# Optimization experiments

Hardware: AMD Instinct MI355X
Metric: run time of the kernel (lower is better)

The kernel has to match this reference:

```python
import jax, jax.numpy as jnp
import numpy as np

B, DIM, L = 16, 1024, 1024
EPS = 1e-12  # F.normalize eps


def l2norm(x, axis=1):
    # torch F.normalize: x / clamp_min(||x||_2, eps)
    n = jnp.sqrt(jnp.sum(x * x, axis=axis, keepdims=True))
    return x / jnp.maximum(n, EPS)


def setup_inputs() -> dict:
    key = jax.random.key(0)
    ks = jax.random.split(key, 8)
    inp = {
        "V": jax.random.normal(ks[0], (B, DIM, L), dtype=jnp.float32),
        "T": jax.random.normal(ks[1], (B, DIM, L), dtype=jnp.float32),
    }
    scale = 1.0 / np.sqrt(DIM)
    names = ["WQ1", "WK1", "WV1", "Wq2", "Wk2", "Wv2"]
    for i, nme in enumerate(names):
        inp[nme] = jax.random.normal(ks[2 + i], (DIM, DIM), dtype=jnp.float32) * scale
    return inp


def reference(V, T, WQ1, WK1, WV1, Wq2, Wk2, Wv2):
    # V, T: [B, dim, L]
    T = l2norm(T, axis=1)                      # normalize over feature dim
    Vt = jnp.swapaxes(V, -2, -1)               # [B, L, dim]
    Tt = jnp.swapaxes(T, -2, -1)               # [B, L, dim]

    relu = jax.nn.relu
    q1 = relu(jnp.einsum('bld,ed->ble', Vt, WQ1))
    k1 = relu(jnp.einsum('bld,ed->ble', Tt, WK1))
    v1 = relu(jnp.einsum('bld,ed->ble', Tt, WV1))
    q2 = relu(jnp.einsum('bld,ed->ble', Tt, Wq2))
    k2 = relu(jnp.einsum('bld,ed->ble', Vt, Wk2))
    v2 = relu(jnp.einsum('bld,ed->ble', Vt, Wv2))

    inv_sqrt_d = 1.0 / jnp.sqrt(jnp.asarray(DIM, dtype=q1.dtype))

    s1 = jnp.einsum('bqd,bkd->bqk', q1, k1) * inv_sqrt_d   # [B, Lv, Lt]
    p1 = jax.nn.softmax(s1, axis=1)                        # softmax over query axis (dim=1)
    w1 = jnp.einsum('bqk,bkd->bqd', p1, v1)                # [B, Lv, dim]
    cV = l2norm(V + jnp.swapaxes(w1, -2, -1), axis=1)      # [B, dim, Lv]

    s2 = jnp.einsum('bqd,bkd->bqk', q2, k2) * inv_sqrt_d   # [B, Lt, Lv]
    p2 = jax.nn.softmax(s2, axis=1)
    w2 = jnp.einsum('bqk,bkd->bqd', p2, v2)                # [B, Lt, dim]
    cT = l2norm(T + jnp.swapaxes(w2, -2, -1), axis=1)      # [B, dim, Lt]

    return l2norm(cV + cT, axis=1)
```

## Files before the change

### kernel.cpp

```cpp
#include <hip/hip_runtime.h>

#define L 1024
#define DIM 1024
#define NB 16

typedef unsigned short u16;
typedef __attribute__((ext_vector_type(4))) float f32x4;
typedef __attribute__((ext_vector_type(8))) short s16x8;

__device__ __forceinline__ float bf2f(u16 x){
  union { unsigned u; float f; } c; c.u = ((unsigned)x) << 16; return c.f;
}
__device__ __forceinline__ u16 f2bf(float f){
  union { float f; unsigned u; } c; c.f = f;
  unsigned r = c.u + 0x7fffu + ((c.u >> 16) & 1u);
  return (u16)(r >> 16);
}
__device__ __forceinline__ void gload_lds16(const void* g, void* l){
  __builtin_amdgcn_global_load_lds(
      (const __attribute__((address_space(1))) void*)g,
      (__attribute__((address_space(3))) void*)l, 16, 0, 0);
}

struct WPtrs { const float* p[6]; };

__global__ __launch_bounds__(256) void k_wconv(WPtrs wp, u16* out){
  long idx = (long)blockIdx.x * blockDim.x + threadIdx.x;
  long base = idx * 4;
  int w = (int)(base >> 20);
  long off = base & ((1 << 20) - 1);
  float4 v = *(const float4*)(wp.p[w] + off);
  ushort4 o;
  o.x = f2bf(v.x); o.y = f2bf(v.y); o.z = f2bf(v.z); o.w = f2bf(v.w);
  *(ushort4*)(out + base) = o;
}

__global__ __launch_bounds__(256) void k_transpose(const float* X, u16* Xt, int bo){
  __shared__ u16 tile[64][68];
  int b = blockIdx.y;
  int d0 = (blockIdx.x >> 4) * 64;
  int l0 = (blockIdx.x & 15) * 64;
  const float* Xb = X + (long)(bo + b) * DIM * L;
  u16* Xtb = Xt + (long)b * L * DIM;
  int q = threadIdx.x & 15, g = threadIdx.x >> 4;
  for (int r = g; r < 64; r += 16){
    float4 v = *(const float4*)(Xb + (long)(d0 + r) * L + l0 + q * 4);
    ushort4 h; h.x = f2bf(v.x); h.y = f2bf(v.y); h.z = f2bf(v.z); h.w = f2bf(v.w);
    *(ushort4*)&tile[r][q * 4] = h;
  }
  __syncthreads();
  for (int r = g; r < 64; r += 16){
    ushort4 h;
    h.x = tile[q * 4 + 0][r]; h.y = tile[q * 4 + 1][r];
    h.z = tile[q * 4 + 2][r]; h.w = tile[q * 4 + 3][r];
    *(ushort4*)&Xtb[(long)(l0 + r) * DIM + d0 + q * 4] = h;
  }
}

__global__ __launch_bounds__(256) void k_tnorm(const float* T_, u16* Tnt, float* rT, int bo){
  __shared__ float red[16][16][5];
  __shared__ float rn[64];
  __shared__ u16 tile[64][68];
  int b = blockIdx.y; int l0 = blockIdx.x * 64;
  const float* Tb = T_ + (long)(bo + b) * DIM * L;
  int q = threadIdx.x & 15, g = threadIdx.x >> 4;
  f32x4 ss = {0.f, 0.f, 0.f, 0.f};
  for (int d = g; d < DIM; d += 16){
    float4 v = *(const float4*)(Tb + (long)d * L + l0 + q * 4);
    f32x4 vv = {v.x, v.y, v.z, v.w};
    ss += vv * vv;
  }
  #pragma unroll
  for (int e = 0; e < 4; e++) red[g][q][e] = ss[e];
  __syncthreads();
  if (threadIdx.x < 64){
    int c = threadIdx.x;
    float n = 0.f;
    #pragma unroll
    for (int gg = 0; gg < 16; gg++) n += red[gg][c >> 2][c & 3];
    float r = 1.0f / fmaxf(sqrtf(n), 1e-12f);
    rn[c] = r;
    rT[(long)b * L + l0 + c] = r;
  }
  __syncthreads();
  float r0 = rn[q * 4], r1 = rn[q * 4 + 1], r2 = rn[q * 4 + 2], r3 = rn[q * 4 + 3];
  u16* Tntb = Tnt + (long)b * L * DIM;
  for (int ch = 0; ch < 16; ch++){
    int dbase = ch * 64;
    for (int r = g; r < 64; r += 16){
      float4 v = *(const float4*)(Tb + (long)(dbase + r) * L + l0 + q * 4);
      ushort4 h;
      h.x = f2bf(v.x * r0); h.y = f2bf(v.y * r1);
      h.z = f2bf(v.z * r2); h.w = f2bf(v.w * r3);
      *(ushort4*)&tile[r][q * 4] = h;
    }
    __syncthreads();
    for (int r = g; r < 64; r += 16){
      ushort4 h;
      h.x = tile[q * 4 + 0][r]; h.y = tile[q * 4 + 1][r];
      h.z = tile[q * 4 + 2][r]; h.w = tile[q * 4 + 3][r];
      *(ushort4*)&Tntb[(long)(l0 + r) * DIM + dbase + q * 4] = h;
    }
    __syncthreads();
  }
}


#define PH(slot, mq, nq, LA, LB, STAGE, WAITC) do {                           \
  if (LA){                                                                    \
    _Pragma("unroll")                                                         \
    for (int f = 0; f < 4; f++){                                              \
      av[f][0] = *(const s16x8*)&lds[(slot)*16384 + arow + (mq)*4096 + f*1024 + cko0]; \
      av[f][1] = *(const s16x8*)&lds[(slot)*16384 + arow + (mq)*4096 + f*1024 + cko1]; \
    }                                                                         \
  }                                                                           \
  if (LB){                                                                    \
    _Pragma("unroll")                                                         \
    for (int g2 = 0; g2 < 2; g2++){                                           \
      bv[nq][g2][0] = *(const s16x8*)&lds[32768 + (slot)*16384 + brow + (nq)*2048 + g2*1024 + cko0]; \
      bv[nq][g2][1] = *(const s16x8*)&lds[32768 + (slot)*16384 + brow + (nq)*2048 + g2*1024 + cko1]; \
    }                                                                         \
  }                                                                           \
  STAGE;                                                                      \
  WAITC;                                                                      \
  __builtin_amdgcn_s_barrier();                                               \
  asm volatile("s_waitcnt lgkmcnt(0)" ::: "memory");                          \
  __builtin_amdgcn_sched_barrier(0);                                          \
  __builtin_amdgcn_s_setprio(1);                                              \
  _Pragma("unroll")                                                           \
  for (int f = 0; f < 4; f++)                                                 \
    _Pragma("unroll")                                                         \
    for (int g2 = 0; g2 < 2; g2++){                                           \
      acc[(mq)*4+f][(nq)*2+g2] = __builtin_amdgcn_mfma_f32_16x16x32_bf16(     \
          av[f][0], bv[nq][g2][0], acc[(mq)*4+f][(nq)*2+g2], 0, 0, 0);        \
      acc[(mq)*4+f][(nq)*2+g2] = __builtin_amdgcn_mfma_f32_16x16x32_bf16(     \
          av[f][1], bv[nq][g2][1], acc[(mq)*4+f][(nq)*2+g2], 0, 0, 0);        \
    }                                                                         \
  __builtin_amdgcn_s_setprio(0);                                              \
  __builtin_amdgcn_s_barrier();                                               \
} while(0)

template<int EPI>
__global__ __launch_bounds__(512, 2) void k_gemm2(const u16* A, const u16* B, u16* C,
                                                  long sA_, long sB_, long sC_,
                                                  const float* Zp, float scale){
  constexpr int K = 1024, NN = 1024, NT = K / 64, NIT = NT / 2;
  __shared__ u16 lds[65536];

  int tid = threadIdx.x;
  int w = tid >> 6, l = tid & 63;
  int wr = w >> 2, wc = w & 3;
  int lr = l & 15, cb = l >> 4;

  int nwg = gridDim.x, cpx = nwg >> 3;
  int swz = (blockIdx.x & 7) * cpx + (blockIdx.x >> 3);
  int batch = swz >> 4;
  int tile = swz & 15;
  int bm = (tile >> 2) * 256, bn = (tile & 3) * 256;

  const u16* Ab = A + (long)batch * sA_ + (long)bm * K;
  const u16* Bb = B + (long)batch * sB_ + (long)bn * K;

  int arow = (wr * 128 + lr) * 64;
  int brow = (wc * 64 + lr) * 64;
  int cko0 = ((cb) ^ (lr & 7)) * 8;
  int cko1 = ((4 + cb) ^ (lr & 7)) * 8;

  int srow8 = l >> 3;
  int schunk = (l & 7) ^ (l >> 3);

  auto stA = [&](int slot, int t, int q){
    #pragma unroll
    for (int j = 0; j < 2; j++){
      int wb = w * 2 + j;
      int gr = ((wb >> 3) * 128) + ((wb & 7) * 8) + q * 64;
      gload_lds16(Ab + (long)(gr + srow8) * K + t * 64 + schunk * 8,
                  (u16*)lds + slot * 16384 + gr * 64);
    }
  };
  auto stB = [&](int slot, int t, int q){
    #pragma unroll
    for (int j = 0; j < 2; j++){
      int wb = w * 2 + j;
      int gr = ((wb >> 2) * 64) + ((wb & 3) * 8) + q * 32;
      gload_lds16(Bb + (long)(gr + srow8) * K + t * 64 + schunk * 8,
                  (u16*)lds + 32768 + slot * 16384 + gr * 64);
    }
  };

  f32x4 acc[8][4] = {};
  s16x8 av[4][2];
  s16x8 bv[2][2][2];

  stA(0, 0, 0); stB(0, 0, 0); stA(0, 0, 1); stB(0, 0, 1);
  stA(1, 1, 0); stB(1, 1, 0);
  asm volatile("s_waitcnt vmcnt(4)" ::: "memory");
  __builtin_amdgcn_s_barrier();

  #pragma unroll 1
  for (int i = 0; i < NIT - 1; ++i){
    int t1 = 2 * i + 1, t2 = 2 * i + 2, t3 = 2 * i + 3;
    PH(0, 0, 0, 1, 1, stA(1, t1, 1), (void)0);
    PH(0, 0, 1, 0, 1, stB(1, t1, 1), (void)0);
    PH(0, 1, 0, 1, 0, stA(0, t2, 0), (void)0);
    PH(0, 1, 1, 0, 0, stB(0, t2, 0), asm volatile("s_waitcnt vmcnt(4)" ::: "memory"));
    PH(1, 0, 0, 1, 1, stA(0, t2, 1), (void)0);
    PH(1, 0, 1, 0, 1, stB(0, t2, 1), (void)0);
    PH(1, 1, 0, 1, 0, stA(1, t3, 0), (void)0);
    PH(1, 1, 1, 0, 0, stB(1, t3, 0), asm volatile("s_waitcnt vmcnt(4)" ::: "memory"));
  }
  {
    int t1 = NT - 1;
    PH(0, 0, 0, 1, 1, stA(1, t1, 1), (void)0);
    PH(0, 0, 1, 0, 1, stB(1, t1, 1), (void)0);
    PH(0, 1, 0, 1, 0, (void)0, (void)0);
    PH(0, 1, 1, 0, 0, (void)0, asm volatile("s_waitcnt vmcnt(0)" ::: "memory"));
    PH(1, 0, 0, 1, 1, (void)0, (void)0);
    PH(1, 0, 1, 0, 1, (void)0, (void)0);
    PH(1, 1, 0, 1, 0, (void)0, (void)0);
    PH(1, 1, 1, 0, 0, (void)0, (void)0);
  }

  float iz[4];
  if (EPI == 2){
    #pragma unroll
    for (int j = 0; j < 4; j++)
      iz[j] = Zp[(long)batch * NN + bn + wc * 64 + j * 16 + lr];
  }
  u16* Cb = C + (long)batch * sC_;
  int cb4 = cb * 4;
  #pragma unroll
  for (int ai = 0; ai < 8; ai++)
    #pragma unroll
    for (int j = 0; j < 4; j++)
      #pragma unroll
      for (int r = 0; r < 4; r++){
        float v = acc[ai][j][r];
        if (EPI == 0) v = fmaxf(v, 0.f);
        else if (EPI == 1) v = __expf(v * scale);
        else if (EPI == 2) v = fmaxf(v, 0.f) * iz[j];
        int row = bm + wr * 128 + ai * 16 + cb4 + r;
        int col = bn + wc * 64 + j * 16 + lr;
        Cb[(long)row * NN + col] = f2bf(v);
      }
}

__global__ __launch_bounds__(256) void k_colsum(const u16* E, float* invZ){
  __shared__ float red[32][8][9];
  int b = blockIdx.y; int k0 = blockIdx.x * 64;
  const u16* Eb = E + (long)b * L * L + k0;
  int co = threadIdx.x & 7, g = threadIdx.x >> 3;
  float z[8] = {0.f, 0.f, 0.f, 0.f, 0.f, 0.f, 0.f, 0.f};
  for (int qq = g; qq < L; qq += 32){
    s16x8 h = *(const s16x8*)(Eb + (long)qq * L + co * 8);
    #pragma unroll
    for (int e = 0; e < 8; e++) z[e] += bf2f((u16)h[e]);
  }
  #pragma unroll
  for (int e = 0; e < 8; e++) red[g][co][e] = z[e];
  __syncthreads();
  if (threadIdx.x < 64){
    int c = threadIdx.x;
    float s = 0.f;
    #pragma unroll
    for (int gg = 0; gg < 32; gg++) s += red[gg][c >> 3][c & 7];
    invZ[(long)b * L + k0 + c] = 1.0f / s;
  }
}

__global__ __launch_bounds__(512) void k_final(const float* V, const float* T_,
                                               const float* rT, const u16* w1t,
                                               const u16* w2t, float* out, int bo){
  __shared__ float red[8][8][12];
  __shared__ float fac[3][32];
  int b = blockIdx.y;
  int c0 = blockIdx.x * 32;
  long gbase = (long)(bo + b) * DIM * L + c0;
  long lbase = (long)b * DIM * L + c0;
  int tid = threadIdx.x;
  int cq = tid & 7, g = tid >> 3, w = tid >> 6;
  int coff = cq * 4;
  float4 rt4 = *(const float4*)(rT + (long)b * L + c0 + coff);
  f32x4 rtv = {rt4.x, rt4.y, rt4.z, rt4.w};
  f32x4 s1 = {0.f,0.f,0.f,0.f}, s2 = {0.f,0.f,0.f,0.f}, s12 = {0.f,0.f,0.f,0.f};
  for (int d = g; d < DIM; d += 64){
    long o = (long)d * L + coff;
    float4 v = *(const float4*)(V + gbase + o);
    float4 t = *(const float4*)(T_ + gbase + o);
    ushort4 w1 = *(const ushort4*)(w1t + lbase + o);
    ushort4 w2 = *(const ushort4*)(w2t + lbase + o);
    f32x4 a = {v.x + bf2f(w1.x), v.y + bf2f(w1.y), v.z + bf2f(w1.z), v.w + bf2f(w1.w)};
    f32x4 tt = {t.x, t.y, t.z, t.w};
    f32x4 bb = tt * rtv;
    bb[0] += bf2f(w2.x); bb[1] += bf2f(w2.y); bb[2] += bf2f(w2.z); bb[3] += bf2f(w2.w);
    s1 += a * a; s2 += bb * bb; s12 += a * bb;
  }
  #pragma unroll
  for (int m = 8; m <= 32; m <<= 1){
    #pragma unroll
    for (int e = 0; e < 4; e++){
      s1[e]  += __shfl_xor(s1[e],  m);
      s2[e]  += __shfl_xor(s2[e],  m);
      s12[e] += __shfl_xor(s12[e], m);
    }
  }
  if ((tid & 63) < 8){
    #pragma unroll
    for (int e = 0; e < 4; e++){
      red[w][cq][e]     = s1[e];
      red[w][cq][4 + e] = s2[e];
      red[w][cq][8 + e] = s12[e];
    }
  }
  __syncthreads();
  if (tid < 96){
    int q = tid / 12, s = tid % 12;
    float a2 = 0.f;
    #pragma unroll
    for (int ww = 0; ww < 8; ww++) a2 += red[ww][q][s];
    red[0][q][s] = a2;
  }
  __syncthreads();
  if (tid < 32){
    int c = tid, q = c >> 2, e = c & 3;
    float n1 = red[0][q][e];
    float n2 = red[0][q][4 + e];
    float cc = red[0][q][8 + e];
    float rn1 = 1.f / fmaxf(sqrtf(n1), 1e-12f);
    float rn2 = 1.f / fmaxf(sqrtf(n2), 1e-12f);
    float n3 = n1 * rn1 * rn1 + 2.f * cc * rn1 * rn2 + n2 * rn2 * rn2;
    float rn3 = 1.f / fmaxf(sqrtf(n3), 1e-12f);
    fac[0][c] = rn1; fac[1][c] = rn2; fac[2][c] = rn3;
  }
  __syncthreads();
  f32x4 f1, f2, f3;
  #pragma unroll
  for (int e = 0; e < 4; e++){
    f1[e] = fac[0][coff + e]; f2[e] = fac[1][coff + e]; f3[e] = fac[2][coff + e];
  }
  for (int d = g; d < DIM; d += 64){
    long o = (long)d * L + coff;
    float4 v = *(const float4*)(V + gbase + o);
    float4 t = *(const float4*)(T_ + gbase + o);
    ushort4 w1 = *(const ushort4*)(w1t + lbase + o);
    ushort4 w2 = *(const ushort4*)(w2t + lbase + o);
    f32x4 a = {v.x + bf2f(w1.x), v.y + bf2f(w1.y), v.z + bf2f(w1.z), v.w + bf2f(w1.w)};
    f32x4 tt = {t.x, t.y, t.z, t.w};
    f32x4 bb = tt * rtv;
    bb[0] += bf2f(w2.x); bb[1] += bf2f(w2.y); bb[2] += bf2f(w2.z); bb[3] += bf2f(w2.w);
    f32x4 r = (a * f1 + bb * f2) * f3;
    float4 st = {r[0], r[1], r[2], r[3]};
    *(float4*)(out + gbase + o) = st;
  }
}

extern "C" void kernel_launch(void* const* d_in, const int* in_sizes, int n_in,
                              void* d_out, int out_size, void* d_ws, size_t ws_size,
                              hipStream_t stream) {
  const float* V = (const float*)d_in[0];
  const float* T = (const float*)d_in[1];
  char* ws = (char*)d_ws;
  const long MB = 1 << 20;
  float* out = (float*)d_out;

  int G = NB;
  while (G > 1 && (size_t)((13 + 14 * (long)G) * MB) > ws_size) G >>= 1;

  u16*   Wb   = (u16*)(ws);
  float* rT   = (float*)(ws + 12 * MB);
  float* invZ = (float*)(ws + 12 * MB + 512 * 1024);
  char*  bufs = ws + 13 * MB;
  long   BUF  = (long)G * 2 * MB;
  u16* Vt  = (u16*)(bufs);
  u16* Tnt = (u16*)(bufs + 1 * BUF);
  u16* qb  = (u16*)(bufs + 2 * BUF);
  u16* kb  = (u16*)(bufs + 3 * BUF);
  u16* Eb  = (u16*)(bufs + 4 * BUF);
  u16* w1b = (u16*)(bufs + 5 * BUF);
  u16* w2b = (u16*)(bufs + 6 * BUF);

  WPtrs wp;
  for (int i = 0; i < 6; i++) wp.p[i] = (const float*)d_in[2 + i];
  const u16* WQ1 = Wb + 0L * MB; const u16* WK1 = Wb + 1L * MB;
  const u16* WV1 = Wb + 2L * MB; const u16* Wq2 = Wb + 3L * MB;
  const u16* Wk2 = Wb + 4L * MB; const u16* Wv2 = Wb + 5L * MB;

  long LD = (long)L * DIM, LL = (long)L * L;
  const float invsq = 0.03125f;

  k_wconv<<<6144, 256, 0, stream>>>(wp, Wb);

  for (int bo = 0; bo < NB; bo += G){
    int ng = 16 * G;
    k_transpose<<<dim3(256, G), 256, 0, stream>>>(V, Vt, bo);
    k_tnorm<<<dim3(16, G), 256, 0, stream>>>(T, Tnt, rT, bo);

    k_gemm2<0><<<ng, 512, 0, stream>>>(Vt,  WQ1, qb, LD, 0, LD, nullptr, 0.f);
    k_gemm2<0><<<ng, 512, 0, stream>>>(Tnt, WK1, kb, LD, 0, LD, nullptr, 0.f);
    k_gemm2<1><<<ng, 512, 0, stream>>>(qb, kb, Eb, LD, LD, LL, nullptr, invsq);
    k_colsum<<<dim3(16, G), 256, 0, stream>>>(Eb, invZ);
    k_gemm2<2><<<ng, 512, 0, stream>>>(WV1, Tnt, qb, 0, LD, LD, invZ, 0.f);
    k_gemm2<3><<<ng, 512, 0, stream>>>(qb, Eb, w1b, LD, LL, LD, nullptr, 0.f);

    k_gemm2<0><<<ng, 512, 0, stream>>>(Tnt, Wq2, qb, LD, 0, LD, nullptr, 0.f);
    k_gemm2<0><<<ng, 512, 0, stream>>>(Vt,  Wk2, kb, LD, 0, LD, nullptr, 0.f);
    k_gemm2<1><<<ng, 512, 0, stream>>>(qb, kb, Eb, LD, LD, LL, nullptr, invsq);
    k_colsum<<<dim3(16, G), 256, 0, stream>>>(Eb, invZ);
    k_gemm2<2><<<ng, 512, 0, stream>>>(Wv2, Vt, qb, 0, LD, LD, invZ, 0.f);
    k_gemm2<3><<<ng, 512, 0, stream>>>(qb, Eb, w2b, LD, LL, LD, nullptr, 0.f);

    k_final<<<dim3(32, G), 512, 0, stream>>>(V, T, rT, w1b, w2b, out, bo);
  }
}
```

Before: 569.1 us.

## Batch independent GEMMs into grouped launches and split softmax normalization

Replaces the twelve sequential per-branch GEMM launches with three grouped launches. A descriptor table lets one kernel run four independent matrix products, such as both attention branches' projections, at once. The 1/Z column normalization moves out of the GEMM epilogue into a separate elementwise pass over the value matrices, and colsum and k_final are widened to cover both branches or more columns per block. The aim is to fill the GPU better with more tiles per launch and cut launch count. In exchange it needs more workspace, turns the epilogue branch into a runtime check, and adds an extra read-modify-write pass over v1 and v2.

```diff
diff --git a/kernel.cpp b/kernel.cpp
--- a/kernel.cpp
+++ b/kernel.cpp
@@ -105,6 +105,13 @@
   }
 }
 
+
+struct GemmDesc {
+  const u16* A[4]; const u16* B[4]; u16* C[4];
+  long sA[4], sB[4], sC[4];
+  int epi[4];
+  float scale;
+};
 
 #define PH(slot, mq, nq, LA, LB, STAGE, WAITC) do {                           \
   if (LA){                                                                    \
@@ -140,10 +147,7 @@
   __builtin_amdgcn_s_barrier();                                               \
 } while(0)
 
-template<int EPI>
-__global__ __launch_bounds__(512, 2) void k_gemm2(const u16* A, const u16* B, u16* C,
-                                                  long sA_, long sB_, long sC_,
-                                                  const float* Zp, float scale){
+__global__ __launch_bounds__(512, 2) void k_gemmM(GemmDesc gd, int shift){
   constexpr int K = 1024, NN = 1024, NT = K / 64, NIT = NT / 2;
   __shared__ u16 lds[65536];
 
@@ -154,12 +158,15 @@
 
   int nwg = gridDim.x, cpx = nwg >> 3;
   int swz = (blockIdx.x & 7) * cpx + (blockIdx.x >> 3);
-  int batch = swz >> 4;
-  int tile = swz & 15;
+  int mat = swz >> shift;
+  int local = swz & ((1 << shift) - 1);
+  int batch = local >> 4;
+  int tile = local & 15;
   int bm = (tile >> 2) * 256, bn = (tile & 3) * 256;
 
-  const u16* Ab = A + (long)batch * sA_ + (long)bm * K;
-  const u16* Bb = B + (long)batch * sB_ + (long)bn * K;
+  const u16* Ab = gd.A[mat] + (long)batch * gd.sA[mat] + (long)bm * K;
+  const u16* Bb = gd.B[mat] + (long)batch * gd.sB[mat] + (long)bn * K;
+  int epi = gd.epi[mat];
 
   int arow = (wr * 128 + lr) * 64;
   int brow = (wc * 64 + lr) * 64;
@@ -221,13 +228,8 @@
     PH(1, 1, 1, 0, 0, (void)0, (void)0);
   }
 
-  float iz[4];
-  if (EPI == 2){
-    #pragma unroll
-    for (int j = 0; j < 4; j++)
-      iz[j] = Zp[(long)batch * NN + bn + wc * 64 + j * 16 + lr];
-  }
-  u16* Cb = C + (long)batch * sC_;
+  u16* Cb = gd.C[mat] + (long)batch * gd.sC[mat];
+  float sc = gd.scale;
   int cb4 = cb * 4;
   #pragma unroll
   for (int ai = 0; ai < 8; ai++)
@@ -236,19 +238,22 @@
       #pragma unroll
       for (int r = 0; r < 4; r++){
         float v = acc[ai][j][r];
-        if (EPI == 0) v = fmaxf(v, 0.f);
-        else if (EPI == 1) v = __expf(v * scale);
-        else if (EPI == 2) v = fmaxf(v, 0.f) * iz[j];
+        if (epi == 0) v = fmaxf(v, 0.f);
+        else if (epi == 1) v = __expf(v * sc);
         int row = bm + wr * 128 + ai * 16 + cb4 + r;
         int col = bn + wc * 64 + j * 16 + lr;
         Cb[(long)row * NN + col] = f2bf(v);
       }
 }
 
-__global__ __launch_bounds__(256) void k_colsum(const u16* E, float* invZ){
+__global__ __launch_bounds__(256) void k_colsum(const u16* E1, const u16* E2,
+                                                float* iz1, float* iz2){
   __shared__ float red[32][8][9];
-  int b = blockIdx.y; int k0 = blockIdx.x * 64;
-  const u16* Eb = E + (long)b * L * L + k0;
+  int side = blockIdx.x >> 4;
+  int k0 = (blockIdx.x & 15) * 64;
+  int b = blockIdx.y;
+  const u16* Eb = (side ? E2 : E1) + (long)b * L * L + k0;
+  float* izp = (side ? iz2 : iz1) + (long)b * L + k0;
   int co = threadIdx.x & 7, g = threadIdx.x >> 3;
   float z[8] = {0.f, 0.f, 0.f, 0.f, 0.f, 0.f, 0.f, 0.f};
   for (int qq = g; qq < L; qq += 32){
@@ -264,21 +269,44 @@
     float s = 0.f;
     #pragma unroll
     for (int gg = 0; gg < 32; gg++) s += red[gg][c >> 3][c & 7];
-    invZ[(long)b * L + k0 + c] = 1.0f / s;
-  }
-}
-
-__global__ __launch_bounds__(512) void k_final(const float* V, const float* T_,
-                                               const float* rT, const u16* w1t,
-                                               const u16* w2t, float* out, int bo){
-  __shared__ float red[8][8][12];
-  __shared__ float fac[3][32];
+    izp[c] = 1.0f / s;
+  }
+}
+
+__global__ __launch_bounds__(256) void k_zapply(u16* v1, u16* v2,
+                                                const float* iz1, const float* iz2){
+  int side = blockIdx.y;
+  u16* v = side ? v2 : v1;
+  const float* izp = side ? iz2 : iz1;
+  long base = ((long)blockIdx.x * 256 + threadIdx.x) * 8;
+  int batch = (int)(base >> 20);
+  int k = (int)(base & 1023);
+  s16x8 h = *(const s16x8*)(v + base);
+  const float* z = izp + (long)batch * 1024 + k;
+  float4 z0 = *(const float4*)z;
+  float4 z1 = *(const float4*)(z + 4);
+  s16x8 o;
+  o[0] = (short)f2bf(bf2f((u16)h[0]) * z0.x);
+  o[1] = (short)f2bf(bf2f((u16)h[1]) * z0.y);
+  o[2] = (short)f2bf(bf2f((u16)h[2]) * z0.z);
+  o[3] = (short)f2bf(bf2f((u16)h[3]) * z0.w);
+  o[4] = (short)f2bf(bf2f((u16)h[4]) * z1.x);
+  o[5] = (short)f2bf(bf2f((u16)h[5]) * z1.y);
+  o[6] = (short)f2bf(bf2f((u16)h[6]) * z1.z);
+  o[7] = (short)f2bf(bf2f((u16)h[7]) * z1.w);
+  *(s16x8*)(v + base) = o;
+}
+
+__global__ __launch_bounds__(1024) void k_final(const float* V, const float* T_,
+                                                const float* rT, const u16* w1t,
+                                                const u16* w2t, float* out, int bo){
+  __shared__ float red[64][16][13];
+  __shared__ float fac[3][64];
   int b = blockIdx.y;
-  int c0 = blockIdx.x * 32;
+  int c0 = blockIdx.x * 64;
   long gbase = (long)(bo + b) * DIM * L + c0;
   long lbase = (long)b * DIM * L + c0;
-  int tid = threadIdx.x;
-  int cq = tid & 7, g = tid >> 3, w = tid >> 6;
+  int cq = threadIdx.x & 15, g = threadIdx.x >> 4;
   int coff = cq * 4;
   float4 rt4 = *(const float4*)(rT + (long)b * L + c0 + coff);
   f32x4 rtv = {rt4.x, rt4.y, rt4.z, rt4.w};
@@ -296,36 +324,25 @@
     s1 += a * a; s2 += bb * bb; s12 += a * bb;
   }
   #pragma unroll
-  for (int m = 8; m <= 32; m <<= 1){
-    #pragma unroll
-    for (int e = 0; e < 4; e++){
-      s1[e]  += __shfl_xor(s1[e],  m);
-      s2[e]  += __shfl_xor(s2[e],  m);
-      s12[e] += __shfl_xor(s12[e], m);
-    }
-  }
-  if ((tid & 63) < 8){
-    #pragma unroll
-    for (int e = 0; e < 4; e++){
-      red[w][cq][e]     = s1[e];
-      red[w][cq][4 + e] = s2[e];
-      red[w][cq][8 + e] = s12[e];
-    }
-  }
-  __syncthreads();
-  if (tid < 96){
-    int q = tid / 12, s = tid % 12;
-    float a2 = 0.f;
-    #pragma unroll
-    for (int ww = 0; ww < 8; ww++) a2 += red[ww][q][s];
-    red[0][q][s] = a2;
-  }
-  __syncthreads();
-  if (tid < 32){
-    int c = tid, q = c >> 2, e = c & 3;
-    float n1 = red[0][q][e];
-    float n2 = red[0][q][4 + e];
-    float cc = red[0][q][8 + e];
+  for (int e = 0; e < 4; e++){
+    red[g][cq][e] = s1[e];
+    red[g][cq][4 + e] = s2[e];
+    red[g][cq][8 + e] = s12[e];
+  }
+  __syncthreads();
+  if (threadIdx.x < 192){
+    int q = threadIdx.x / 12, s = threadIdx.x % 12;
+    float acc = 0.f;
+    #pragma unroll 8
+    for (int gg = 0; gg < 64; gg++) acc += red[gg][q][s];
+    red[0][q][s] = acc;
+  }
+  __syncthreads();
+  if (threadIdx.x < 64){
+    int c = threadIdx.x;
+    float n1 = red[0][c >> 2][c & 3];
+    float n2 = red[0][c >> 2][4 + (c & 3)];
+    float cc = red[0][c >> 2][8 + (c & 3)];
     float rn1 = 1.f / fmaxf(sqrtf(n1), 1e-12f);
     float rn2 = 1.f / fmaxf(sqrtf(n2), 1e-12f);
     float n3 = n1 * rn1 * rn1 + 2.f * cc * rn1 * rn2 + n2 * rn2 * rn2;
@@ -364,20 +381,27 @@
   float* out = (float*)d_out;
 
   int G = NB;
-  while (G > 1 && (size_t)((13 + 14 * (long)G) * MB) > ws_size) G >>= 1;
-
-  u16*   Wb   = (u16*)(ws);
-  float* rT   = (float*)(ws + 12 * MB);
-  float* invZ = (float*)(ws + 12 * MB + 512 * 1024);
+  while (G > 1 && (size_t)((13 + 24 * (long)G) * MB) > ws_size) G >>= 1;
+  int shift = 4 + (31 - __builtin_clz((unsigned)G));
+
+  u16*   Wb  = (u16*)(ws);
+  float* rT  = (float*)(ws + 12 * MB);
+  float* iz1 = (float*)(ws + 12 * MB + 256 * 1024);
+  float* iz2 = (float*)(ws + 12 * MB + 512 * 1024);
   char*  bufs = ws + 13 * MB;
   long   BUF  = (long)G * 2 * MB;
-  u16* Vt  = (u16*)(bufs);
-  u16* Tnt = (u16*)(bufs + 1 * BUF);
-  u16* qb  = (u16*)(bufs + 2 * BUF);
-  u16* kb  = (u16*)(bufs + 3 * BUF);
-  u16* Eb  = (u16*)(bufs + 4 * BUF);
-  u16* w1b = (u16*)(bufs + 5 * BUF);
-  u16* w2b = (u16*)(bufs + 6 * BUF);
+  u16* Vt  = (u16*)(bufs + 0  * BUF);
+  u16* Tnt = (u16*)(bufs + 1  * BUF);
+  u16* q1  = (u16*)(bufs + 2  * BUF);
+  u16* k1  = (u16*)(bufs + 3  * BUF);
+  u16* q2  = (u16*)(bufs + 4  * BUF);
+  u16* k2  = (u16*)(bufs + 5  * BUF);
+  u16* E1  = (u16*)(bufs + 6  * BUF);
+  u16* E2  = (u16*)(bufs + 7  * BUF);
+  u16* v1  = (u16*)(bufs + 8  * BUF);
+  u16* v2  = (u16*)(bufs + 9  * BUF);
+  u16* w1b = (u16*)(bufs + 10 * BUF);
+  u16* w2b = (u16*)(bufs + 11 * BUF);
 
   WPtrs wp;
   for (int i = 0; i < 6; i++) wp.p[i] = (const float*)d_in[2 + i];
@@ -385,30 +409,44 @@
   const u16* WV1 = Wb + 2L * MB; const u16* Wq2 = Wb + 3L * MB;
   const u16* Wk2 = Wb + 4L * MB; const u16* Wv2 = Wb + 5L * MB;
 
-  long LD = (long)L * DIM, LL = (long)L * L;
+  long LD = (long)L * DIM;
   const float invsq = 0.03125f;
 
+  GemmDesc g1;
+  g1.A[0] = Vt;  g1.B[0] = WQ1; g1.C[0] = q1;
+  g1.A[1] = Tnt; g1.B[1] = WK1; g1.C[1] = k1;
+  g1.A[2] = Tnt; g1.B[2] = Wq2; g1.C[2] = q2;
+  g1.A[3] = Vt;  g1.B[3] = Wk2; g1.C[3] = k2;
+  for (int i = 0; i < 4; i++){ g1.sA[i] = LD; g1.sB[i] = 0; g1.sC[i] = LD; g1.epi[i] = 0; }
+  g1.scale = 0.f;
+
+  GemmDesc g2;
+  g2.A[0] = q1;  g2.B[0] = k1;  g2.C[0] = E1; g2.sA[0] = LD; g2.sB[0] = LD; g2.sC[0] = LD; g2.epi[0] = 1;
+  g2.A[1] = q2;  g2.B[1] = k2;  g2.C[1] = E2; g2.sA[1] = LD; g2.sB[1] = LD; g2.sC[1] = LD; g2.epi[1] = 1;
+  g2.A[2] = WV1; g2.B[2] = Tnt; g2.C[2] = v1; g2.sA[2] = 0;  g2.sB[2] = LD; g2.sC[2] = LD; g2.epi[2] = 0;
+  g2.A[3] = Wv2; g2.B[3] = Vt;  g2.C[3] = v2; g2.sA[3] = 0;  g2.sB[3] = LD; g2.sC[3] = LD; g2.epi[3] = 0;
+  g2.scale = invsq;
+
+  GemmDesc g3;
+  g3.A[0] = v1; g3.B[0] = E1; g3.C[0] = w1b;
+  g3.A[1] = v2; g3.B[1] = E2; g3.C[1] = w2b;
+  g3.A[2] = v1; g3.B[2] = E1; g3.C[2] = w1b;
+  g3.A[3] = v1; g3.B[3] = E1; g3.C[3] = w1b;
+  for (int i = 0; i < 4; i++){ g3.sA[i] = LD; g3.sB[i] = LD; g3.sC[i] = LD; g3.epi[i] = 3; }
+  g3.scale = 0.f;
+
   k_wconv<<<6144, 256, 0, stream>>>(wp, Wb);
 
   for (int bo = 0; bo < NB; bo += G){
-    int ng = 16 * G;
     k_transpose<<<dim3(256, G), 256, 0, stream>>>(V, Vt, bo);
     k_tnorm<<<dim3(16, G), 256, 0, stream>>>(T, Tnt, rT, bo);
 
-    k_gemm2<0><<<ng, 512, 0, stream>>>(Vt,  WQ1, qb, LD, 0, LD, nullptr, 0.f);
-    k_gemm2<0><<<ng, 512, 0, stream>>>(Tnt, WK1, kb, LD, 0, LD, nullptr, 0.f);
-    k_gemm2<1><<<ng, 512, 0, stream>>>(qb, kb, Eb, LD, LD, LL, nullptr, invsq);
-    k_colsum<<<dim3(16, G), 256, 0, stream>>>(Eb, invZ);
-    k_gemm2<2><<<ng, 512, 0, stream>>>(WV1, Tnt, qb, 0, LD, LD, invZ, 0.f);
-    k_gemm2<3><<<ng, 512, 0, stream>>>(qb, Eb, w1b, LD, LL, LD, nullptr, 0.f);
-
-    k_gemm2<0><<<ng, 512, 0, stream>>>(Tnt, Wq2, qb, LD, 0, LD, nullptr, 0.f);
-    k_gemm2<0><<<ng, 512, 0, stream>>>(Vt,  Wk2, kb, LD, 0, LD, nullptr, 0.f);
-    k_gemm2<1><<<ng, 512, 0, stream>>>(qb, kb, Eb, LD, LD, LL, nullptr, invsq);
-    k_colsum<<<dim3(16, G), 256, 0, stream>>>(Eb, invZ);
-    k_gemm2<2><<<ng, 512, 0, stream>>>(Wv2, Vt, qb, 0, LD, LD, invZ, 0.f);
-    k_gemm2<3><<<ng, 512, 0, stream>>>(qb, Eb, w2b, LD, LL, LD, nullptr, 0.f);
-
-    k_final<<<dim3(32, G), 512, 0, stream>>>(V, T, rT, w1b, w2b, out, bo);
-  }
-}
+    k_gemmM<<<4 * 16 * G, 512, 0, stream>>>(g1, shift);
+    k_gemmM<<<4 * 16 * G, 512, 0, stream>>>(g2, shift);
+    k_colsum<<<dim3(32, G), 256, 0, stream>>>(E1, E2, iz1, iz2);
+    k_zapply<<<dim3(G * 512, 2), 256, 0, stream>>>(v1, v2, iz1, iz2);
+    k_gemmM<<<2 * 16 * G, 512, 0, stream>>>(g3, shift);
+
+    k_final<<<dim3(16, G), 1024, 0, stream>>>(V, T, rT, w1b, w2b, out, bo);
+  }
+}
```

Measured after the change: 654.5 us. +15.0%, slower.
